# Kernel optimization log

Measured on AMD Instinct MI355X. Metric: run time of the kernel, lower is better.

Reference implementation:

```python
import jax, jax.numpy as jnp
import numpy as np

ALPHA = 1.0  # initial_alpha; forward uses self.alpha which stays at init value

def setup_inputs() -> dict:
    key = jax.random.key(0)
    k1, k2, k3, k4 = jax.random.split(key, 4)
    B, T, N, C, K = 8, 32, 2048, 64, 32
    R_seq = jax.random.normal(k1, (B, T, N, C), dtype=jnp.float32)
    W = jax.random.normal(k2, (K, C), dtype=jnp.float32) * (1.0 / np.sqrt(C))
    b = jax.random.normal(k3, (K,), dtype=jnp.float32) * 0.01
    cent = jax.random.normal(k4, (K, C), dtype=jnp.float32)
    centroids = cent / jnp.linalg.norm(cent, axis=1, keepdims=True)  # xavier + L2-normalize rows
    return {"R_seq": R_seq, "W": W, "b": b, "centroids": centroids}

def reference(R_seq, W, b, centroids):
    B, T, N, C = R_seq.shape
    K = centroids.shape[0]
    r = R_seq.reshape(B * T, N, C)                       # (BT, N, C)
    logits = (jnp.einsum('mnc,kc->mnk', r, W) + b) * ALPHA
    a = jax.nn.softmax(logits, axis=-1)                  # (BT, N, K)
    # NetVLAD algebraic decomposition: v_k = a_k^T r - (sum_n a_nk) * c_k
    v = jnp.einsum('mnk,mnc->mkc', a, r) - a.sum(axis=1)[:, :, None] * centroids[None]
    return v.reshape(B, T, K, C)
```

## Files before the change

kernel.cpp:

```cpp
#include <hip/hip_runtime.h>
#include <stdint.h>

typedef __attribute__((ext_vector_type(8))) short bf16x8;
typedef __attribute__((ext_vector_type(4))) short bf16x4;
typedef __attribute__((ext_vector_type(4))) float f32x4;

#define WAVES 4
#define R_STRIDE 72
#define A_STRIDE 40
#define R_LDS_SHORTS (32 * R_STRIDE)
#define A_LDS_SHORTS (32 * A_STRIDE)
#define WAVE_LDS (R_LDS_SHORTS + A_LDS_SHORTS)
#define VB_STRIDE 68
#define NITER 4
#define WS_STRIDE 2080

static __device__ __forceinline__ unsigned short f2bf(float f) {
    union { float f; unsigned int i; } x; x.f = f;
    unsigned int i = x.i;
    return (unsigned short)((i + 0x7FFFu + ((i >> 16) & 1u)) >> 16);
}

static __device__ __forceinline__ bf16x8 cvt8(float4 a, float4 b) {
    bf16x8 r;
    r[0] = (short)f2bf(a.x); r[1] = (short)f2bf(a.y);
    r[2] = (short)f2bf(a.z); r[3] = (short)f2bf(a.w);
    r[4] = (short)f2bf(b.x); r[5] = (short)f2bf(b.y);
    r[6] = (short)f2bf(b.z); r[7] = (short)f2bf(b.w);
    return r;
}

static __device__ __forceinline__ float row_sum16(float x) {
    union fi { float f; int i; };
    fi a, b; a.f = x;
    b.i = __builtin_amdgcn_mov_dpp(a.i, 0x128, 0xf, 0xf, false); a.f += b.f;
    b.i = __builtin_amdgcn_mov_dpp(a.i, 0x124, 0xf, 0xf, false); a.f += b.f;
    b.i = __builtin_amdgcn_mov_dpp(a.i, 0x122, 0xf, 0xf, false); a.f += b.f;
    b.i = __builtin_amdgcn_mov_dpp(a.i, 0x121, 0xf, 0xf, false); a.f += b.f;
    return a.f;
}


__global__ __launch_bounds__(256, 4)
void netvlad_partial(const float* __restrict__ R,
                     const float* __restrict__ W,
                     const float* __restrict__ bias,
                     float* __restrict__ ws)
{
    __shared__ short smem[WAVES * WAVE_LDS];
    __shared__ float suma_buf[2][32];

    const int tid  = threadIdx.x;
    const int wave = tid >> 6;
    const int lane = tid & 63;
    const int l15  = lane & 15;
    const int quad = lane >> 4;
    const int bid  = blockIdx.x;
    const int m    = bid >> 2;
    const int h    = bid & 3;

    short* r_lds = smem + wave * WAVE_LDS;
    short* a_lds = r_lds + R_LDS_SHORTS;

    const float* Rm = R + ((size_t)m * 2048 + (size_t)h * 512) * 64;

    bf16x8 wf[2][2];
#pragma unroll
    for (int kt = 0; kt < 2; ++kt)
#pragma unroll
        for (int cc = 0; cc < 2; ++cc) {
            const float* wp = W + (kt*16 + l15)*64 + cc*32 + quad*8;
            wf[kt][cc] = cvt8(*(const float4*)wp, *(const float4*)(wp + 4));
        }

    float bval[2];
    bval[0] = bias[l15];
    bval[1] = bias[16 + l15];

    f32x4 acc[2][4];
#pragma unroll
    for (int kt = 0; kt < 2; ++kt)
#pragma unroll
        for (int ct = 0; ct < 4; ++ct)
            acc[kt][ct] = (f32x4){0.f, 0.f, 0.f, 0.f};
    float suma[2] = {0.f, 0.f};

#pragma unroll
    for (int it = 0; it < NITER; ++it) {
        const int n0 = it * (WAVES * 32) + wave * 32;

        bf16x8 af[2][2];
#pragma unroll
        for (int s = 0; s < 2; ++s) {
            const int g = (s*2 + (l15 >> 3)) & 3;
#pragma unroll
            for (int cc = 0; cc < 2; ++cc) {
                const float* rp = Rm + (size_t)(n0 + s*16 + l15)*64 + cc*32 + quad*8;
                const float4 x0 = *(const float4*)rp;
                const float4 x1 = *(const float4*)(rp + 4);
                af[s][cc] = cvt8(x0, x1);
                const int c0s = (cc*32 + quad*8) ^ (g << 4);
                *(bf16x8*)(r_lds + (s*16 + l15)*R_STRIDE + c0s) = af[s][cc];
            }
        }

        f32x4 d1[2][2];
#pragma unroll
        for (int s = 0; s < 2; ++s)
#pragma unroll
            for (int kt = 0; kt < 2; ++kt) {
                f32x4 d = (f32x4){0.f, 0.f, 0.f, 0.f};
                d = __builtin_amdgcn_mfma_f32_16x16x32_bf16(af[s][0], wf[kt][0], d, 0, 0, 0);
                d = __builtin_amdgcn_mfma_f32_16x16x32_bf16(af[s][1], wf[kt][1], d, 0, 0, 0);
                d1[s][kt] = d;
            }

#pragma unroll
        for (int s = 0; s < 2; ++s) {
            bf16x4 p0, p1;
            float a0s = 0.f, a1s = 0.f;
#pragma unroll
            for (int r = 0; r < 4; ++r) {
                float l0 = d1[s][0][r] + bval[0];
                float l1 = d1[s][1][r] + bval[1];
                float e0 = __expf(l0);
                float e1 = __expf(l1);
                float ss = row_sum16(e0 + e1);
                float rs = __builtin_amdgcn_rcpf(ss);
                float a0 = e0 * rs, a1 = e1 * rs;
                a0s += a0; a1s += a1;
                p0[r] = (short)f2bf(a0);
                p1[r] = (short)f2bf(a1);
            }
            suma[0] += a0s; suma[1] += a1s;
            *(bf16x4*)(a_lds + l15*A_STRIDE        + s*16 + quad*4) = p0;
            *(bf16x4*)(a_lds + (16 + l15)*A_STRIDE + s*16 + quad*4) = p1;
        }

        bf16x8 a2[2];
#pragma unroll
        for (int kt = 0; kt < 2; ++kt)
            a2[kt] = *(bf16x8*)(a_lds + (kt*16 + l15)*A_STRIDE + quad*8);

#pragma unroll
        for (int ct = 0; ct < 4; ++ct) {
            const short* bp = r_lds + (quad*8)*R_STRIDE + ((ct ^ quad) << 4) + l15;
            bf16x8 b2;
#pragma unroll
            for (int j = 0; j < 8; ++j)
                b2[j] = bp[j*R_STRIDE];
#pragma unroll
            for (int kt = 0; kt < 2; ++kt)
                acc[kt][ct] = __builtin_amdgcn_mfma_f32_16x16x32_bf16(a2[kt], b2, acc[kt][ct], 0, 0, 0);
        }
    }

#pragma unroll
    for (int kt = 0; kt < 2; ++kt) {
        suma[kt] += __shfl_xor(suma[kt], 16);
        suma[kt] += __shfl_xor(suma[kt], 32);
    }

    float* vbuf = (float*)smem;
    __syncthreads();
#pragma unroll
    for (int step = 2; step >= 1; step >>= 1) {
        if (wave >= step && wave < 2*step) {
            float* dst = vbuf + (wave - step) * (32 * VB_STRIDE);
#pragma unroll
            for (int kt = 0; kt < 2; ++kt)
#pragma unroll
                for (int ct = 0; ct < 4; ++ct)
#pragma unroll
                    for (int r = 0; r < 4; ++r)
                        dst[(kt*16 + quad*4 + r)*VB_STRIDE + ct*16 + l15] = acc[kt][ct][r];
            if (lane < 16) {
                suma_buf[wave - step][lane]      = suma[0];
                suma_buf[wave - step][lane + 16] = suma[1];
            }
        }
        __syncthreads();
        if (wave < step) {
            const float* src = vbuf + wave * (32 * VB_STRIDE);
#pragma unroll
            for (int kt = 0; kt < 2; ++kt)
#pragma unroll
                for (int ct = 0; ct < 4; ++ct)
#pragma unroll
                    for (int r = 0; r < 4; ++r)
                        acc[kt][ct][r] += src[(kt*16 + quad*4 + r)*VB_STRIDE + ct*16 + l15];
            suma[0] += suma_buf[wave][l15];
            suma[1] += suma_buf[wave][l15 + 16];
        }
        __syncthreads();
    }

    if (wave == 0) {
        float* wp = ws + (size_t)bid * WS_STRIDE;
#pragma unroll
        for (int kt = 0; kt < 2; ++kt)
#pragma unroll
            for (int r = 0; r < 4; ++r) {
                const int k = kt*16 + quad*4 + r;
#pragma unroll
                for (int ct = 0; ct < 4; ++ct)
                    wp[k*64 + ct*16 + l15] = acc[kt][ct][r];
            }
        if (lane < 16) {
            wp[2048 + lane]      = suma[0];
            wp[2048 + 16 + lane] = suma[1];
        }
    }
}

__global__ __launch_bounds__(512)
void netvlad_combine(const float* __restrict__ ws,
                     const float* __restrict__ cent,
                     float* __restrict__ out)
{
    const int m   = blockIdx.x;
    const int tid = threadIdx.x;
    const float* p0 = ws + (size_t)(4*m) * WS_STRIDE;
    const float* p1 = p0 + WS_STRIDE;
    const float* p2 = p1 + WS_STRIDE;
    const float* p3 = p2 + WS_STRIDE;

    const int k  = tid >> 4;
    const int c0 = (tid & 15) << 2;
    const float s = (p0[2048 + k] + p1[2048 + k]) + (p2[2048 + k] + p3[2048 + k]);

    const int off = k*64 + c0;
    const float4 v0 = *(const float4*)(p0 + off);
    const float4 v1 = *(const float4*)(p1 + off);
    const float4 v2 = *(const float4*)(p2 + off);
    const float4 v3 = *(const float4*)(p3 + off);
    const float4 cv = *(const float4*)(cent + off);
    float4 o;
    o.x = (v0.x + v1.x) + (v2.x + v3.x) - s * cv.x;
    o.y = (v0.y + v1.y) + (v2.y + v3.y) - s * cv.y;
    o.z = (v0.z + v1.z) + (v2.z + v3.z) - s * cv.z;
    o.w = (v0.w + v1.w) + (v2.w + v3.w) - s * cv.w;
    *(float4*)(out + (size_t)m * 2048 + off) = o;
}

extern "C" void kernel_launch(void* const* d_in, const int* in_sizes, int n_in,
                              void* d_out, int out_size, void* d_ws, size_t ws_size,
                              hipStream_t stream) {
    (void)in_sizes; (void)n_in; (void)out_size; (void)ws_size;
    const float* R = (const float*)d_in[0];
    const float* W = (const float*)d_in[1];
    const float* b = (const float*)d_in[2];
    const float* c = (const float*)d_in[3];
    float* out = (float*)d_out;
    float* ws  = (float*)d_ws;

    hipLaunchKernelGGL(netvlad_partial, dim3(1024), dim3(256), 0, stream, R, W, b, ws);
    hipLaunchKernelGGL(netvlad_combine, dim3(256), dim3(512), 0, stream, ws, c, out);
}
```

Measured before the change: 228.3 us.

## Split N into eight chunks per frame and stage W in shared memory

The partial kernel now splits each frame's 2048 points into eight chunks instead of four. That doubles the grid to 2048 blocks, and the combine kernel now sums eight partial results instead of four. W is converted once into swizzled LDS and reloaded per MFMA instead of being held in registers. The main loop is no longer unrolled, and the cluster-assignment MFMA and softmax are interleaved per sub-tile to cut register pressure, with the occupancy hint lowered to 2 blocks per CU. This aims to raise memory-level parallelism on a bandwidth-bound read, at the cost of twice the workspace traffic and extra LDS reads of W.

After: 206.7 us. -9.5%, faster.

```diff
diff --git a/kernel.cpp b/kernel.cpp
--- a/kernel.cpp
+++ b/kernel.cpp
@@ -11,8 +11,10 @@
 #define R_LDS_SHORTS (32 * R_STRIDE)
 #define A_LDS_SHORTS (32 * A_STRIDE)
 #define WAVE_LDS (R_LDS_SHORTS + A_LDS_SHORTS)
+#define W_LDS_OFF (WAVES * WAVE_LDS)
+#define SMEM_SHORTS (W_LDS_OFF + 2048)
 #define VB_STRIDE 68
-#define NITER 4
+#define NITER 2
 #define WS_STRIDE 2080
 
 static __device__ __forceinline__ unsigned short f2bf(float f) {
@@ -40,15 +42,13 @@
     return a.f;
 }
 
-
-__global__ __launch_bounds__(256, 4)
+__global__ __launch_bounds__(256, 2)
 void netvlad_partial(const float* __restrict__ R,
                      const float* __restrict__ W,
                      const float* __restrict__ bias,
                      float* __restrict__ ws)
 {
-    __shared__ short smem[WAVES * WAVE_LDS];
-    __shared__ float suma_buf[2][32];
+    __shared__ short smem[SMEM_SHORTS];
 
     const int tid  = threadIdx.x;
     const int wave = tid >> 6;
@@ -56,21 +56,24 @@
     const int l15  = lane & 15;
     const int quad = lane >> 4;
     const int bid  = blockIdx.x;
-    const int m    = bid >> 2;
-    const int h    = bid & 3;
+    const int m    = bid >> 3;
+    const int h    = bid & 7;
 
     short* r_lds = smem + wave * WAVE_LDS;
     short* a_lds = r_lds + R_LDS_SHORTS;
-
-    const float* Rm = R + ((size_t)m * 2048 + (size_t)h * 512) * 64;
-
-    bf16x8 wf[2][2];
+    short* w_lds = smem + W_LDS_OFF;
+
+    const float* Rm = R + ((size_t)m * 2048 + (size_t)h * 256) * 64;
+
 #pragma unroll
     for (int kt = 0; kt < 2; ++kt)
 #pragma unroll
         for (int cc = 0; cc < 2; ++cc) {
-            const float* wp = W + (kt*16 + l15)*64 + cc*32 + quad*8;
-            wf[kt][cc] = cvt8(*(const float4*)wp, *(const float4*)(wp + 4));
+            const int k = kt*16 + l15;
+            const int c = cc*32 + quad*8;
+            const float* wp = W + k*64 + c;
+            bf16x8 wv = cvt8(*(const float4*)wp, *(const float4*)(wp + 4));
+            *(bf16x8*)(w_lds + k*64 + (c ^ ((k & 7) << 3))) = wv;
         }
 
     float bval[2];
@@ -85,44 +88,43 @@
             acc[kt][ct] = (f32x4){0.f, 0.f, 0.f, 0.f};
     float suma[2] = {0.f, 0.f};
 
-#pragma unroll
+#pragma unroll 1
     for (int it = 0; it < NITER; ++it) {
         const int n0 = it * (WAVES * 32) + wave * 32;
 
-        bf16x8 af[2][2];
 #pragma unroll
         for (int s = 0; s < 2; ++s) {
             const int g = (s*2 + (l15 >> 3)) & 3;
-#pragma unroll
-            for (int cc = 0; cc < 2; ++cc) {
-                const float* rp = Rm + (size_t)(n0 + s*16 + l15)*64 + cc*32 + quad*8;
-                const float4 x0 = *(const float4*)rp;
-                const float4 x1 = *(const float4*)(rp + 4);
-                af[s][cc] = cvt8(x0, x1);
-                const int c0s = (cc*32 + quad*8) ^ (g << 4);
-                *(bf16x8*)(r_lds + (s*16 + l15)*R_STRIDE + c0s) = af[s][cc];
-            }
-        }
-
-        f32x4 d1[2][2];
-#pragma unroll
-        for (int s = 0; s < 2; ++s)
+            bf16x8 af0, af1;
+            {
+                const float* rp = Rm + (size_t)(n0 + s*16 + l15)*64 + quad*8;
+                af0 = cvt8(*(const float4*)rp, *(const float4*)(rp + 4));
+                *(bf16x8*)(r_lds + (s*16 + l15)*R_STRIDE + ((quad*8) ^ (g << 4))) = af0;
+            }
+            {
+                const float* rp = Rm + (size_t)(n0 + s*16 + l15)*64 + 32 + quad*8;
+                af1 = cvt8(*(const float4*)rp, *(const float4*)(rp + 4));
+                *(bf16x8*)(r_lds + (s*16 + l15)*R_STRIDE + ((32 + quad*8) ^ (g << 4))) = af1;
+            }
+
+            f32x4 d1s[2];
 #pragma unroll
             for (int kt = 0; kt < 2; ++kt) {
+                const int k = kt*16 + l15;
+                const bf16x8 w0 = *(const bf16x8*)(w_lds + k*64 + ((quad*8)      ^ ((k & 7) << 3)));
+                const bf16x8 w1 = *(const bf16x8*)(w_lds + k*64 + ((32 + quad*8) ^ ((k & 7) << 3)));
                 f32x4 d = (f32x4){0.f, 0.f, 0.f, 0.f};
-                d = __builtin_amdgcn_mfma_f32_16x16x32_bf16(af[s][0], wf[kt][0], d, 0, 0, 0);
-                d = __builtin_amdgcn_mfma_f32_16x16x32_bf16(af[s][1], wf[kt][1], d, 0, 0, 0);
-                d1[s][kt] = d;
-            }
-
-#pragma unroll
-        for (int s = 0; s < 2; ++s) {
+                d = __builtin_amdgcn_mfma_f32_16x16x32_bf16(af0, w0, d, 0, 0, 0);
+                d = __builtin_amdgcn_mfma_f32_16x16x32_bf16(af1, w1, d, 0, 0, 0);
+                d1s[kt] = d;
+            }
+
             bf16x4 p0, p1;
             float a0s = 0.f, a1s = 0.f;
 #pragma unroll
             for (int r = 0; r < 4; ++r) {
-                float l0 = d1[s][0][r] + bval[0];
-                float l1 = d1[s][1][r] + bval[1];
+                float l0 = d1s[0][r] + bval[0];
+                float l1 = d1s[1][r] + bval[1];
                 float e0 = __expf(l0);
                 float e1 = __expf(l1);
                 float ss = row_sum16(e0 + e1);
@@ -162,6 +164,7 @@
     }
 
     float* vbuf = (float*)smem;
+    float* suma_buf = (float*)(smem + W_LDS_OFF);
     __syncthreads();
 #pragma unroll
     for (int step = 2; step >= 1; step >>= 1) {
@@ -175,8 +178,8 @@
                     for (int r = 0; r < 4; ++r)
                         dst[(kt*16 + quad*4 + r)*VB_STRIDE + ct*16 + l15] = acc[kt][ct][r];
             if (lane < 16) {
-                suma_buf[wave - step][lane]      = suma[0];
-                suma_buf[wave - step][lane + 16] = suma[1];
+                suma_buf[(wave - step)*32 + lane]      = suma[0];
+                suma_buf[(wave - step)*32 + lane + 16] = suma[1];
             }
         }
         __syncthreads();
@@ -189,8 +192,8 @@
 #pragma unroll
                     for (int r = 0; r < 4; ++r)
                         acc[kt][ct][r] += src[(kt*16 + quad*4 + r)*VB_STRIDE + ct*16 + l15];
-            suma[0] += suma_buf[wave][l15];
-            suma[1] += suma_buf[wave][l15 + 16];
+            suma[0] += suma_buf[wave*32 + l15];
+            suma[1] += suma_buf[wave*32 + l15 + 16];
         }
         __syncthreads();
     }
@@ -220,26 +223,28 @@
 {
     const int m   = blockIdx.x;
     const int tid = threadIdx.x;
-    const float* p0 = ws + (size_t)(4*m) * WS_STRIDE;
-    const float* p1 = p0 + WS_STRIDE;
-    const float* p2 = p1 + WS_STRIDE;
-    const float* p3 = p2 + WS_STRIDE;
+    const float* pb = ws + (size_t)(8*m) * WS_STRIDE;
 
     const int k  = tid >> 4;
     const int c0 = (tid & 15) << 2;
-    const float s = (p0[2048 + k] + p1[2048 + k]) + (p2[2048 + k] + p3[2048 + k]);
-
     const int off = k*64 + c0;
-    const float4 v0 = *(const float4*)(p0 + off);
-    const float4 v1 = *(const float4*)(p1 + off);
-    const float4 v2 = *(const float4*)(p2 + off);
-    const float4 v3 = *(const float4*)(p3 + off);
+
+    float s = 0.f;
+    float4 v = {0.f, 0.f, 0.f, 0.f};
+#pragma unroll
+    for (int i = 0; i < 8; ++i) {
+        const float* p = pb + (size_t)i * WS_STRIDE;
+        s += p[2048 + k];
+        const float4 vi = *(const float4*)(p + off);
+        v.x += vi.x; v.y += vi.y; v.z += vi.z; v.w += vi.w;
+    }
+
     const float4 cv = *(const float4*)(cent + off);
     float4 o;
-    o.x = (v0.x + v1.x) + (v2.x + v3.x) - s * cv.x;
-    o.y = (v0.y + v1.y) + (v2.y + v3.y) - s * cv.y;
-    o.z = (v0.z + v1.z) + (v2.z + v3.z) - s * cv.z;
-    o.w = (v0.w + v1.w) + (v2.w + v3.w) - s * cv.w;
+    o.x = v.x - s * cv.x;
+    o.y = v.y - s * cv.y;
+    o.z = v.z - s * cv.z;
+    o.w = v.w - s * cv.w;
     *(float4*)(out + (size_t)m * 2048 + off) = o;
 }
 
@@ -254,6 +259,6 @@
     float* out = (float*)d_out;
     float* ws  = (float*)d_ws;
 
-    hipLaunchKernelGGL(netvlad_partial, dim3(1024), dim3(256), 0, stream, R, W, b, ws);
+    hipLaunchKernelGGL(netvlad_partial, dim3(2048), dim3(256), 0, stream, R, W, b, ws);
     hipLaunchKernelGGL(netvlad_combine, dim3(256), dim3(512), 0, stream, ws, c, out);
 }
```
